# Performance work log

Measured on AMD Instinct MI355X. Metric: run time of the kernel, lower is better.

The kernel has to match this reference:

```python
import jax, jax.numpy as jnp
import numpy as np

B, T, C = 8, 2048, 1024
HEAD = 64

def setup_inputs() -> dict:
    key = jax.random.key(0)
    k1, k2 = jax.random.split(key)
    x = jax.random.normal(k1, (B, T, C), dtype=jnp.float32)
    W_qkv = jax.random.normal(k2, (C, 3 * HEAD), dtype=jnp.float32) * (C ** -0.5)
    return {"x": x, "W_qkv": W_qkv}

def reference(x, W_qkv):
    # qkv projection (bias-free Linear): [B,T,3*HEAD]
    qkv = x @ W_qkv
    q, k, v = jnp.split(qkv, 3, axis=-1)  # each [B,T,HEAD]
    # scaled dot-product scores [B,T,T]
    dots = jnp.einsum('btd,bsd->bts', q, k) * (HEAD ** -0.5)
    # causal mask (tril == keep)
    Tq = x.shape[1]
    causal = jnp.tril(jnp.ones((Tq, Tq), dtype=bool))
    dots = jnp.where(causal, dots, -jnp.inf)
    attn = jax.nn.softmax(dots, axis=-1)
    # dropout p=0.0 (eval) -> identity
    out = jnp.einsum('bts,bsd->btd', attn, v)  # [B,T,HEAD]
    return out
```

## Files before the change

### kernel.cpp

```cpp
#include <hip/hip_runtime.h>
#include <stdint.h>

#define NB 8
#define NT 2048
#define NC 1024
#define HD 64

typedef __attribute__((ext_vector_type(8)))  short s16x8;
typedef __attribute__((ext_vector_type(4)))  float f32x4;
typedef __attribute__((ext_vector_type(16))) float f32x16;

__device__ inline ushort f2b(float f) {
    union { float f; uint32_t u; } c; c.f = f;
    uint32_t u = c.u;
    uint32_t r = (u + 0x7fffu + ((u >> 16) & 1u)) >> 16;
    return (ushort)r;
}

__device__ inline uint32_t cvt_pk_bf16(float lo, float hi) {
    uint32_t r;
    asm volatile("v_cvt_pk_bf16_f32 %0, %1, %2" : "=v"(r) : "v"(lo), "v"(hi));
    return r;
}

__global__ __launch_bounds__(256) void wprep(const float* __restrict__ W,
                                             ushort* __restrict__ wt) {
    int tid = blockIdx.x * 256 + threadIdx.x;
    int n = tid >> 10;
    int k = tid & 1023;
    float v = W[k * 192 + n];
    if (n < 64) v *= 0.125f * 1.4426950408889634f;
    wt[n * 1024 + k] = f2b(v);
}

#define ASTR 40
#define WSTR 40

__global__ __launch_bounds__(256) void qkv_gemm(const float* __restrict__ x,
                                                const ushort* __restrict__ wt,
                                                ushort* __restrict__ qs,
                                                ushort* __restrict__ kk,
                                                ushort* __restrict__ vt) {
    __shared__ ushort Al[2][64 * ASTR];
    __shared__ ushort Wl[2][192 * WSTR];

    const int tid = threadIdx.x;
    const int wv  = tid >> 6;
    const int ln  = tid & 63;
    const int r16 = ln & 15;
    const int hi4 = ln >> 4;
    const int row0 = blockIdx.x * 64;

    const int arow = tid >> 2;
    const int ac   = tid & 3;
    const float* xsrc = x + (size_t)(row0 + arow) * NC + ac * 8;

    int wcol[3], wc[3];
    const ushort* wsrc[3];
#pragma unroll
    for (int j = 0; j < 3; ++j) {
        int q = tid + 256 * j;
        wcol[j] = q >> 2;
        wc[j]   = q & 3;
        wsrc[j] = wt + (size_t)wcol[j] * 1024 + wc[j] * 8;
    }

    f32x4 acc[4][3];
#pragma unroll
    for (int i = 0; i < 4; ++i)
#pragma unroll
        for (int j = 0; j < 3; ++j)
#pragma unroll
            for (int e = 0; e < 4; ++e) acc[i][j][e] = 0.f;

    {
        float4 xa = *(const float4*)(xsrc);
        float4 xb = *(const float4*)(xsrc + 4);
        uint4 wr0 = *(const uint4*)(wsrc[0]);
        uint4 wr1 = *(const uint4*)(wsrc[1]);
        uint4 wr2 = *(const uint4*)(wsrc[2]);
        union { ushort u[8]; s16x8 v; } pk;
        pk.u[0] = f2b(xa.x); pk.u[1] = f2b(xa.y); pk.u[2] = f2b(xa.z); pk.u[3] = f2b(xa.w);
        pk.u[4] = f2b(xb.x); pk.u[5] = f2b(xb.y); pk.u[6] = f2b(xb.z); pk.u[7] = f2b(xb.w);
        *(s16x8*)(&Al[0][arow * ASTR + ac * 8]) = pk.v;
        *(uint4*)(&Wl[0][wcol[0] * WSTR + wc[0] * 8]) = wr0;
        *(uint4*)(&Wl[0][wcol[1] * WSTR + wc[1] * 8]) = wr1;
        *(uint4*)(&Wl[0][wcol[2] * WSTR + wc[2] * 8]) = wr2;
    }
    __syncthreads();

    int buf = 0;
    for (int t = 0; t < 32; ++t) {
        float4 nxa, nxb; uint4 nw0, nw1, nw2;
        if (t < 31) {
            int k0 = (t + 1) * 32;
            nxa = *(const float4*)(xsrc + k0);
            nxb = *(const float4*)(xsrc + k0 + 4);
            nw0 = *(const uint4*)(wsrc[0] + k0);
            nw1 = *(const uint4*)(wsrc[1] + k0);
            nw2 = *(const uint4*)(wsrc[2] + k0);
        }

        s16x8 af[4], bfr[3];
#pragma unroll
        for (int mi = 0; mi < 4; ++mi)
            af[mi] = *(const s16x8*)(&Al[buf][(mi * 16 + r16) * ASTR + hi4 * 8]);
#pragma unroll
        for (int ni = 0; ni < 3; ++ni) {
            int col = (wv * 3 + ni) * 16 + r16;
            bfr[ni] = *(const s16x8*)(&Wl[buf][col * WSTR + hi4 * 8]);
        }
#pragma unroll
        for (int mi = 0; mi < 4; ++mi)
#pragma unroll
            for (int ni = 0; ni < 3; ++ni)
                acc[mi][ni] = __builtin_amdgcn_mfma_f32_16x16x32_bf16(
                    af[mi], bfr[ni], acc[mi][ni], 0, 0, 0);

        if (t < 31) {
            int nb = buf ^ 1;
            union { ushort u[8]; s16x8 v; } pk;
            pk.u[0] = f2b(nxa.x); pk.u[1] = f2b(nxa.y); pk.u[2] = f2b(nxa.z); pk.u[3] = f2b(nxa.w);
            pk.u[4] = f2b(nxb.x); pk.u[5] = f2b(nxb.y); pk.u[6] = f2b(nxb.z); pk.u[7] = f2b(nxb.w);
            *(s16x8*)(&Al[nb][arow * ASTR + ac * 8]) = pk.v;
            *(uint4*)(&Wl[nb][wcol[0] * WSTR + wc[0] * 8]) = nw0;
            *(uint4*)(&Wl[nb][wcol[1] * WSTR + wc[1] * 8]) = nw1;
            *(uint4*)(&Wl[nb][wcol[2] * WSTR + wc[2] * 8]) = nw2;
        }
        __syncthreads();
        buf ^= 1;
    }

    const int b = row0 >> 11;
#pragma unroll
    for (int mi = 0; mi < 4; ++mi) {
#pragma unroll
        for (int ni = 0; ni < 3; ++ni) {
            int nf = wv * 3 + ni;
            int colg = nf * 16 + r16;
            int rbase = row0 + mi * 16 + hi4 * 4;
            f32x4 v = acc[mi][ni];
            if (nf < 4) {
#pragma unroll
                for (int j = 0; j < 4; ++j)
                    qs[(size_t)(rbase + j) * HD + colg] = f2b(v[j]);
            } else if (nf < 8) {
#pragma unroll
                for (int j = 0; j < 4; ++j)
                    kk[(size_t)(rbase + j) * HD + (colg - 64)] = f2b(v[j]);
            } else {
                int d = colg - 128;
                union { ushort4 s; ushort u[4]; } pk;
#pragma unroll
                for (int j = 0; j < 4; ++j) pk.u[j] = f2b(v[j]);
                *(ushort4*)(&vt[((size_t)(b * 64 + d)) * NT + (rbase & (NT - 1))]) = pk.s;
            }
        }
    }
}

__global__ __launch_bounds__(256) void attn(const ushort* __restrict__ qs,
                                            const ushort* __restrict__ kk,
                                            const ushort* __restrict__ vt,
                                            float* __restrict__ out) {
    __shared__ float ob[4][64][33];
    __shared__ float ml[4][2][32];

    const int bid  = blockIdx.x;
    const int b    = bid & 7;
    const int tile = 63 - (bid >> 3);
    const int tid  = threadIdx.x;
    const int wv   = tid >> 6;
    const int l    = tid & 63;
    const int qcol = l & 31;
    const int hi   = l >> 5;
    const int r0   = tile * 32;

    const ushort* qb = qs + ((size_t)(b * NT + r0)) * HD;
    const ushort* kb = kk + (size_t)b * NT * HD;
    const ushort* vb = vt + (size_t)b * HD * NT;

    s16x8 qf[4];
#pragma unroll
    for (int c = 0; c < 4; ++c)
        qf[c] = *(const s16x8*)(qb + (size_t)qcol * HD + c * 16 + hi * 8);

    f32x16 o0, o1;
#pragma unroll
    for (int i = 0; i < 16; ++i) { o0[i] = 0.f; o1[i] = 0.f; }
    float m = -3.0e30f, lsum = 0.f;

    if (wv <= tile) {
        s16x8 kf[4], vf[4];
        {
            const ushort* kr = kb + (size_t)(wv * 32 + qcol) * HD;
#pragma unroll
            for (int c = 0; c < 4; ++c)
                kf[c] = *(const s16x8*)(kr + c * 16 + hi * 8);
#pragma unroll
            for (int dt = 0; dt < 2; ++dt)
#pragma unroll
                for (int kc = 0; kc < 2; ++kc)
                    vf[dt * 2 + kc] = *(const s16x8*)(vb + (size_t)(dt * 32 + qcol) * NT
                                                      + wv * 32 + kc * 16 + hi * 8);
        }

        for (int kt = wv; kt <= tile; kt += 4) {
            f32x16 s;
#pragma unroll
            for (int i = 0; i < 16; ++i) s[i] = 0.f;
#pragma unroll
            for (int c = 0; c < 4; ++c)
                s = __builtin_amdgcn_mfma_f32_32x32x16_bf16(kf[c], qf[c], s, 0, 0, 0);

            s16x8 kfn[4], vfn[4];
            const bool more = (kt + 4 <= tile);
            if (more) {
                const ushort* kr = kb + (size_t)((kt + 4) * 32 + qcol) * HD;
#pragma unroll
                for (int c = 0; c < 4; ++c)
                    kfn[c] = *(const s16x8*)(kr + c * 16 + hi * 8);
#pragma unroll
                for (int dt = 0; dt < 2; ++dt)
#pragma unroll
                    for (int kc = 0; kc < 2; ++kc)
                        vfn[dt * 2 + kc] = *(const s16x8*)(vb + (size_t)(dt * 32 + qcol) * NT
                                                           + (kt + 4) * 32 + kc * 16 + hi * 8);
            }

            const bool diag = (kt == tile);
            float p[16];
#pragma unroll
            for (int r = 0; r < 16; ++r) {
                int klocal = (r & 3) + 8 * (r >> 2) + 4 * hi;
                float sv = s[r];
                if (diag && klocal > qcol) sv = -3.0e30f;
                p[r] = sv;
            }
            float pmax = p[0];
#pragma unroll
            for (int r = 1; r < 16; ++r) pmax = fmaxf(pmax, p[r]);
            pmax = fmaxf(pmax, __shfl_xor(pmax, 32));
            float mnew = fmaxf(m, pmax);
            float corr = exp2f(m - mnew);
            m = mnew;
            float rs = 0.f;
#pragma unroll
            for (int r = 0; r < 16; ++r) { p[r] = exp2f(p[r] - mnew); rs += p[r]; }
            rs += __shfl_xor(rs, 32);
            lsum = lsum * corr + rs;
#pragma unroll
            for (int i = 0; i < 16; ++i) { o0[i] *= corr; o1[i] *= corr; }

#pragma unroll
            for (int kc = 0; kc < 2; ++kc) {
                int pb = kc * 8;
                uint32_t a0 = cvt_pk_bf16(p[pb + 0], p[pb + 1]);
                uint32_t a1 = cvt_pk_bf16(p[pb + 2], p[pb + 3]);
                uint32_t b0 = cvt_pk_bf16(p[pb + 4], p[pb + 5]);
                uint32_t b1 = cvt_pk_bf16(p[pb + 6], p[pb + 7]);
                uint32_t a0x = __shfl_xor(a0, 32);
                uint32_t a1x = __shfl_xor(a1, 32);
                uint32_t b0x = __shfl_xor(b0, 32);
                uint32_t b1x = __shfl_xor(b1, 32);
                union { uint32_t w[4]; s16x8 v; } frag;
                frag.w[0] = hi ? b0x : a0;
                frag.w[1] = hi ? b1x : a1;
                frag.w[2] = hi ? b0  : a0x;
                frag.w[3] = hi ? b1  : a1x;
                o0 = __builtin_amdgcn_mfma_f32_32x32x16_bf16(vf[0 * 2 + kc], frag.v, o0, 0, 0, 0);
                o1 = __builtin_amdgcn_mfma_f32_32x32x16_bf16(vf[1 * 2 + kc], frag.v, o1, 0, 0, 0);
            }

            if (more) {
#pragma unroll
                for (int c = 0; c < 4; ++c) kf[c] = kfn[c];
#pragma unroll
                for (int c = 0; c < 4; ++c) vf[c] = vfn[c];
            }
        }
    }

#pragma unroll
    for (int r = 0; r < 16; ++r) {
        int d = (r & 3) + 8 * (r >> 2) + 4 * hi;
        ob[wv][d][qcol]      = o0[r];
        ob[wv][d + 32][qcol] = o1[r];
    }
    if (hi == 0) {
        ml[wv][0][qcol] = m;
        ml[wv][1][qcol] = lsum;
    }
    __syncthreads();

    const int q  = tid >> 3;
    const int j0 = (tid & 7) * 8;
    float mw[4];
#pragma unroll
    for (int w = 0; w < 4; ++w) mw[w] = ml[w][0][q];
    float M = fmaxf(fmaxf(mw[0], mw[1]), fmaxf(mw[2], mw[3]));
    float sw[4]; float L = 0.f;
#pragma unroll
    for (int w = 0; w < 4; ++w) {
        sw[w] = exp2f(mw[w] - M);
        L += sw[w] * ml[w][1][q];
    }
    float invL = 1.0f / L;
    float vals[8];
#pragma unroll
    for (int j = 0; j < 8; ++j) {
        int d = j0 + j;
        float acc = 0.f;
#pragma unroll
        for (int w = 0; w < 4; ++w) acc += sw[w] * ob[w][d][q];
        vals[j] = acc * invL;
    }
    float* orow = out + ((size_t)(b * NT + r0 + q)) * HD + j0;
    *(float4*)(orow)     = make_float4(vals[0], vals[1], vals[2], vals[3]);
    *(float4*)(orow + 4) = make_float4(vals[4], vals[5], vals[6], vals[7]);
}

extern "C" void kernel_launch(void* const* d_in, const int* in_sizes, int n_in,
                              void* d_out, int out_size, void* d_ws, size_t ws_size,
                              hipStream_t stream) {
    const float* x = (const float*)d_in[0];
    const float* W = (const float*)d_in[1];
    float* out = (float*)d_out;

    ushort* qs = (ushort*)d_ws;
    ushort* kk = qs + (size_t)NB * NT * HD;
    ushort* vt = kk + (size_t)NB * NT * HD;
    ushort* wt = vt + (size_t)NB * NT * HD;

    wprep<<<768, 256, 0, stream>>>(W, wt);
    qkv_gemm<<<256, 256, 0, stream>>>(x, wt, qs, kk, vt);
    attn<<<512, 256, 0, stream>>>(qs, kk, vt, out);
}
```

Baseline: 58.34 us.

## Drop LDS staging in QKV GEMM; load operands directly into registers

Rewrites the QKV projection GEMM so each wave owns 16 rows and all 12 column fragments, loading x and the transposed weights straight from global memory into MFMA operand registers. This removes the shared-memory tiles and their per-iteration barriers, and uses a two-stage register double buffer for prefetch. It also switches x conversion to packed bf16 convert instructions and removes volatile from that asm. In exchange, weight fragments are re-read from global/L2 by every wave instead of being shared through LDS, and register pressure rises sharply (launch bounds set to one block).

```diff
diff --git a/kernel.cpp b/kernel.cpp
--- a/kernel.cpp
+++ b/kernel.cpp
@@ -19,7 +19,7 @@
 
 __device__ inline uint32_t cvt_pk_bf16(float lo, float hi) {
     uint32_t r;
-    asm volatile("v_cvt_pk_bf16_f32 %0, %1, %2" : "=v"(r) : "v"(lo), "v"(hi));
+    asm("v_cvt_pk_bf16_f32 %0, %1, %2" : "=v"(r) : "v"(lo), "v"(hi));
     return r;
 }
 
@@ -33,128 +33,105 @@
     wt[n * 1024 + k] = f2b(v);
 }
 
-#define ASTR 40
-#define WSTR 40
-
-__global__ __launch_bounds__(256) void qkv_gemm(const float* __restrict__ x,
-                                                const ushort* __restrict__ wt,
-                                                ushort* __restrict__ qs,
-                                                ushort* __restrict__ kk,
-                                                ushort* __restrict__ vt) {
-    __shared__ ushort Al[2][64 * ASTR];
-    __shared__ ushort Wl[2][192 * WSTR];
-
+__global__ __launch_bounds__(256, 1) void qkv_gemm(const float* __restrict__ x,
+                                                   const ushort* __restrict__ wt,
+                                                   ushort* __restrict__ qs,
+                                                   ushort* __restrict__ kk,
+                                                   ushort* __restrict__ vt) {
     const int tid = threadIdx.x;
     const int wv  = tid >> 6;
     const int ln  = tid & 63;
     const int r16 = ln & 15;
     const int hi4 = ln >> 4;
     const int row0 = blockIdx.x * 64;
-
-    const int arow = tid >> 2;
-    const int ac   = tid & 3;
-    const float* xsrc = x + (size_t)(row0 + arow) * NC + ac * 8;
-
-    int wcol[3], wc[3];
-    const ushort* wsrc[3];
-#pragma unroll
-    for (int j = 0; j < 3; ++j) {
-        int q = tid + 256 * j;
-        wcol[j] = q >> 2;
-        wc[j]   = q & 3;
-        wsrc[j] = wt + (size_t)wcol[j] * 1024 + wc[j] * 8;
-    }
-
-    f32x4 acc[4][3];
-#pragma unroll
-    for (int i = 0; i < 4; ++i)
-#pragma unroll
-        for (int j = 0; j < 3; ++j)
-#pragma unroll
-            for (int e = 0; e < 4; ++e) acc[i][j][e] = 0.f;
-
-    {
-        float4 xa = *(const float4*)(xsrc);
-        float4 xb = *(const float4*)(xsrc + 4);
-        uint4 wr0 = *(const uint4*)(wsrc[0]);
-        uint4 wr1 = *(const uint4*)(wsrc[1]);
-        uint4 wr2 = *(const uint4*)(wsrc[2]);
-        union { ushort u[8]; s16x8 v; } pk;
-        pk.u[0] = f2b(xa.x); pk.u[1] = f2b(xa.y); pk.u[2] = f2b(xa.z); pk.u[3] = f2b(xa.w);
-        pk.u[4] = f2b(xb.x); pk.u[5] = f2b(xb.y); pk.u[6] = f2b(xb.z); pk.u[7] = f2b(xb.w);
-        *(s16x8*)(&Al[0][arow * ASTR + ac * 8]) = pk.v;
-        *(uint4*)(&Wl[0][wcol[0] * WSTR + wc[0] * 8]) = wr0;
-        *(uint4*)(&Wl[0][wcol[1] * WSTR + wc[1] * 8]) = wr1;
-        *(uint4*)(&Wl[0][wcol[2] * WSTR + wc[2] * 8]) = wr2;
-    }
-    __syncthreads();
-
-    int buf = 0;
-    for (int t = 0; t < 32; ++t) {
-        float4 nxa, nxb; uint4 nw0, nw1, nw2;
-        if (t < 31) {
-            int k0 = (t + 1) * 32;
-            nxa = *(const float4*)(xsrc + k0);
-            nxb = *(const float4*)(xsrc + k0 + 4);
-            nw0 = *(const uint4*)(wsrc[0] + k0);
-            nw1 = *(const uint4*)(wsrc[1] + k0);
-            nw2 = *(const uint4*)(wsrc[2] + k0);
-        }
-
-        s16x8 af[4], bfr[3];
-#pragma unroll
-        for (int mi = 0; mi < 4; ++mi)
-            af[mi] = *(const s16x8*)(&Al[buf][(mi * 16 + r16) * ASTR + hi4 * 8]);
-#pragma unroll
-        for (int ni = 0; ni < 3; ++ni) {
-            int col = (wv * 3 + ni) * 16 + r16;
-            bfr[ni] = *(const s16x8*)(&Wl[buf][col * WSTR + hi4 * 8]);
-        }
-#pragma unroll
-        for (int mi = 0; mi < 4; ++mi)
-#pragma unroll
-            for (int ni = 0; ni < 3; ++ni)
-                acc[mi][ni] = __builtin_amdgcn_mfma_f32_16x16x32_bf16(
-                    af[mi], bfr[ni], acc[mi][ni], 0, 0, 0);
-
-        if (t < 31) {
-            int nb = buf ^ 1;
-            union { ushort u[8]; s16x8 v; } pk;
-            pk.u[0] = f2b(nxa.x); pk.u[1] = f2b(nxa.y); pk.u[2] = f2b(nxa.z); pk.u[3] = f2b(nxa.w);
-            pk.u[4] = f2b(nxb.x); pk.u[5] = f2b(nxb.y); pk.u[6] = f2b(nxb.z); pk.u[7] = f2b(nxb.w);
-            *(s16x8*)(&Al[nb][arow * ASTR + ac * 8]) = pk.v;
-            *(uint4*)(&Wl[nb][wcol[0] * WSTR + wc[0] * 8]) = nw0;
-            *(uint4*)(&Wl[nb][wcol[1] * WSTR + wc[1] * 8]) = nw1;
-            *(uint4*)(&Wl[nb][wcol[2] * WSTR + wc[2] * 8]) = nw2;
-        }
-        __syncthreads();
-        buf ^= 1;
+    const int myrow = row0 + wv * 16 + r16;
+
+    const float* xp = x + (size_t)myrow * NC + hi4 * 8;
+    const ushort* wp[12];
+#pragma unroll
+    for (int nf = 0; nf < 12; ++nf)
+        wp[nf] = wt + (size_t)(nf * 16 + r16) * 1024 + hi4 * 8;
+
+    f32x4 acc[12];
+#pragma unroll
+    for (int i = 0; i < 12; ++i)
+#pragma unroll
+        for (int e = 0; e < 4; ++e) acc[i][e] = 0.f;
+
+    float4 xA0 = *(const float4*)(xp);
+    float4 xA1 = *(const float4*)(xp + 4);
+    float4 xB0 = *(const float4*)(xp + 32);
+    float4 xB1 = *(const float4*)(xp + 36);
+    s16x8 wA[12], wB[12];
+#pragma unroll
+    for (int nf = 0; nf < 12; ++nf) wA[nf] = *(const s16x8*)(wp[nf]);
+#pragma unroll
+    for (int nf = 0; nf < 12; ++nf) wB[nf] = *(const s16x8*)(wp[nf] + 32);
+
+#pragma unroll
+    for (int t = 0; t < 32; t += 2) {
+        {
+            union { uint32_t w[4]; s16x8 v; } pk;
+            pk.w[0] = cvt_pk_bf16(xA0.x, xA0.y);
+            pk.w[1] = cvt_pk_bf16(xA0.z, xA0.w);
+            pk.w[2] = cvt_pk_bf16(xA1.x, xA1.y);
+            pk.w[3] = cvt_pk_bf16(xA1.z, xA1.w);
+            s16x8 a = pk.v;
+            if (t + 2 < 32) {
+                xA0 = *(const float4*)(xp + (t + 2) * 32);
+                xA1 = *(const float4*)(xp + (t + 2) * 32 + 4);
+            }
+#pragma unroll
+            for (int nf = 0; nf < 12; ++nf)
+                acc[nf] = __builtin_amdgcn_mfma_f32_16x16x32_bf16(a, wA[nf], acc[nf], 0, 0, 0);
+            if (t + 2 < 32) {
+#pragma unroll
+                for (int nf = 0; nf < 12; ++nf)
+                    wA[nf] = *(const s16x8*)(wp[nf] + (t + 2) * 32);
+            }
+        }
+        {
+            union { uint32_t w[4]; s16x8 v; } pk;
+            pk.w[0] = cvt_pk_bf16(xB0.x, xB0.y);
+            pk.w[1] = cvt_pk_bf16(xB0.z, xB0.w);
+            pk.w[2] = cvt_pk_bf16(xB1.x, xB1.y);
+            pk.w[3] = cvt_pk_bf16(xB1.z, xB1.w);
+            s16x8 a = pk.v;
+            if (t + 3 < 32) {
+                xB0 = *(const float4*)(xp + (t + 3) * 32);
+                xB1 = *(const float4*)(xp + (t + 3) * 32 + 4);
+            }
+#pragma unroll
+            for (int nf = 0; nf < 12; ++nf)
+                acc[nf] = __builtin_amdgcn_mfma_f32_16x16x32_bf16(a, wB[nf], acc[nf], 0, 0, 0);
+            if (t + 3 < 32) {
+#pragma unroll
+                for (int nf = 0; nf < 12; ++nf)
+                    wB[nf] = *(const s16x8*)(wp[nf] + (t + 3) * 32);
+            }
+        }
     }
 
     const int b = row0 >> 11;
-#pragma unroll
-    for (int mi = 0; mi < 4; ++mi) {
-#pragma unroll
-        for (int ni = 0; ni < 3; ++ni) {
-            int nf = wv * 3 + ni;
-            int colg = nf * 16 + r16;
-            int rbase = row0 + mi * 16 + hi4 * 4;
-            f32x4 v = acc[mi][ni];
-            if (nf < 4) {
-#pragma unroll
-                for (int j = 0; j < 4; ++j)
-                    qs[(size_t)(rbase + j) * HD + colg] = f2b(v[j]);
-            } else if (nf < 8) {
-#pragma unroll
-                for (int j = 0; j < 4; ++j)
-                    kk[(size_t)(rbase + j) * HD + (colg - 64)] = f2b(v[j]);
-            } else {
-                int d = colg - 128;
-                union { ushort4 s; ushort u[4]; } pk;
-#pragma unroll
-                for (int j = 0; j < 4; ++j) pk.u[j] = f2b(v[j]);
-                *(ushort4*)(&vt[((size_t)(b * 64 + d)) * NT + (rbase & (NT - 1))]) = pk.s;
-            }
+    const int rbase = row0 + wv * 16 + hi4 * 4;
+#pragma unroll
+    for (int nf = 0; nf < 12; ++nf) {
+        int colg = nf * 16 + r16;
+        f32x4 v = acc[nf];
+        if (nf < 4) {
+#pragma unroll
+            for (int j = 0; j < 4; ++j)
+                qs[(size_t)(rbase + j) * HD + colg] = f2b(v[j]);
+        } else if (nf < 8) {
+#pragma unroll
+            for (int j = 0; j < 4; ++j)
+                kk[(size_t)(rbase + j) * HD + (colg - 64)] = f2b(v[j]);
+        } else {
+            int d = colg - 128;
+            union { ushort4 s; ushort u[4]; } pk;
+#pragma unroll
+            for (int j = 0; j < 4; ++j) pk.u[j] = f2b(v[j]);
+            *(ushort4*)(&vt[((size_t)(b * 64 + d)) * NT + (rbase & (NT - 1))]) = pk.s;
         }
     }
 }
```

After: 107.0 us. +83.5%, slower.
